# Performance work log

Hardware: AMD Instinct MI355X
Metric: run time of the kernel (lower is better)

The kernel has to match this reference:

```python
import jax, jax.numpy as jnp
import numpy as np

B, T, C, H = 4, 2048, 1024, 16
D = C // H  # head_size = 64


def setup_inputs() -> dict:
    key = jax.random.key(0)
    k1, k2, k3 = jax.random.split(key, 3)
    h = jax.random.normal(k1, (B, T, C), dtype=jnp.float32)
    # additive float mask, [B,1,1,T]; zeros = no padding
    attention_mask = jnp.zeros((B, 1, 1, T), dtype=jnp.float32)
    # learned params (bias=False linears), scaled like default torch init
    w_attn = jax.random.normal(k2, (C, 3 * C), dtype=jnp.float32) / np.sqrt(C)
    w_proj = jax.random.normal(k3, (C, C), dtype=jnp.float32) / np.sqrt(C)
    return {"h": h, "attention_mask": attention_mask, "w_attn": w_attn, "w_proj": w_proj}


def reference(h, attention_mask, w_attn, w_proj):
    # fused QKV projection: [B,T,3C]
    qkv = jnp.einsum("btc,cd->btd", h, w_attn)
    q, k, v = jnp.split(qkv, 3, axis=-1)
    # [B,T,C] -> [B,H,T,D]
    def to_heads(x):
        return x.reshape(B, T, H, D).transpose(0, 2, 1, 3)
    q, k, v = to_heads(q), to_heads(k), to_heads(v)
    # scaled dot-product attention with additive mask (non-causal)
    scale = 1.0 / np.sqrt(D).astype(np.float32)
    scores = jnp.einsum("bhqd,bhkd->bhqk", q, k) * scale + attention_mask
    probs = jax.nn.softmax(scores, axis=-1)
    y = jnp.einsum("bhqk,bhkd->bhqd", probs, v)
    # [B,H,T,D] -> [B,T,C]
    y = y.transpose(0, 2, 1, 3).reshape(B, T, C)
    return jnp.einsum("btc,cd->btd", y, w_proj)
```

## Files before the change

kernel.cpp:

```cpp
#include <hip/hip_runtime.h>
#include <hip/hip_bf16.h>

#define DEV static __device__ __forceinline__

typedef __attribute__((ext_vector_type(4))) float f32x4;
typedef __attribute__((ext_vector_type(16))) float f32x16;
typedef __attribute__((ext_vector_type(8))) short bf16x8;

constexpr int Bb = 4, Ts = 2048, Cc = 1024, Hh = 16, Dd = 64;
constexpr int Mm = Bb * Ts;
constexpr float SCQ = 0.18033688f;

union frag_u {
  bf16x8 f;
  uint2  u2[2];
  ushort us[8];
  uint4  u4;
};

DEV ushort f2bf(float x) {
  union { float f; unsigned u; } v; v.f = x;
  unsigned r = v.u + 0x7FFFu + ((v.u >> 16) & 1u);
  return (ushort)(r >> 16);
}

DEV ushort f2bf_hw(float x) {
  union { __hip_bfloat16 b; ushort u; } cv;
  cv.b = __float2bfloat16(x);
  return cv.u;
}

typedef const __attribute__((address_space(1))) unsigned int gu32;
typedef __attribute__((address_space(3))) unsigned int lu32;
DEV void gload16(const void* g, void* l) {
  __builtin_amdgcn_global_load_lds((gu32*)g, (lu32*)l, 16, 0, 0);
}

DEV void ld_frag16(frag_u& fr, const ushort* lds, int row, int chunk) {
  int off = row * 128 + ((chunk ^ (row & 7)) << 4);
  fr.u4 = *reinterpret_cast<const uint4*>(reinterpret_cast<const char*>(lds) + off);
}
DEV void lds_st64p(ushort* lds, int row, int p, uint2 v) {
  int off = row * 128 + ((((p >> 3) ^ (row & 7)) << 4) | ((2 * p) & 15));
  *reinterpret_cast<uint2*>(reinterpret_cast<char*>(lds) + off) = v;
}

DEV void eW64b(char* E, int row, int col, uint2 v) {
  int off = row * 256 + ((((col >> 3) ^ (row & 15)) << 4) | ((col & 7) * 2));
  *reinterpret_cast<uint2*>(E + off) = v;
}
DEV uint4 eR128b(const char* E, int row, int dc) {
  int off = row * 256 + ((dc ^ (row & 15)) << 4);
  return *reinterpret_cast<const uint4*>(E + off);
}

__global__ __launch_bounds__(256) void cvt_kernel(const float* __restrict__ in,
                                                  ushort* __restrict__ out, int n4) {
  for (int i = blockIdx.x * blockDim.x + threadIdx.x; i < n4;
       i += gridDim.x * blockDim.x) {
    float4 v = reinterpret_cast<const float4*>(in)[i];
    ushort4 o;
    o.x = f2bf(v.x); o.y = f2bf(v.y); o.z = f2bf(v.z); o.w = f2bf(v.w);
    reinterpret_cast<ushort4*>(out)[i] = o;
  }
}

__global__ __launch_bounds__(256) void expmask_kernel(const float* __restrict__ m,
                                                      float* __restrict__ em, int n) {
  int i = blockIdx.x * blockDim.x + threadIdx.x;
  if (i < n) em[i] = __expf(m[i]);
}

__global__ __launch_bounds__(256) void transpose_cvt(const float* __restrict__ in,
                                                     ushort* __restrict__ out,
                                                     int R, int Ccols) {
  __shared__ float tile[32][33];
  int c0 = blockIdx.x * 32, r0 = blockIdx.y * 32;
  int tx = threadIdx.x & 31, ty = threadIdx.x >> 5;
#pragma unroll
  for (int i = 0; i < 4; ++i) {
    int r = ty + i * 8;
    tile[r][tx] = in[(size_t)(r0 + r) * Ccols + c0 + tx];
  }
  __syncthreads();
#pragma unroll
  for (int i = 0; i < 4; ++i) {
    int r = ty + i * 8;
    out[(size_t)(c0 + r) * R + r0 + tx] = f2bf(tile[tx][r]);
  }
}

template <int EPI>
__global__ __launch_bounds__(256) void gemm_bt(const ushort* __restrict__ A,
                                               const ushort* __restrict__ Bt,
                                               int M, int N, int K,
                                               float* __restrict__ Cf,
                                               ushort* __restrict__ Qb,
                                               ushort* __restrict__ Kb,
                                               ushort* __restrict__ Vb,
                                               const float* __restrict__ expm) {
  __shared__ ushort Lds[2][128 * 64];
  __shared__ float evals[128];
  ushort* Al = Lds[0];
  ushort* Bl = Lds[1];
  const int tid = threadIdx.x;
  const int lane = tid & 63, wid = tid >> 6;
  const int l31 = lane & 31, lh = lane >> 5;
  const int wr = wid >> 1, wc = wid & 1;
  const int m0 = blockIdx.y * 128, n0 = blockIdx.x * 128;

  if (EPI == 1 && tid < 128)
    evals[tid] = expm[(size_t)(m0 >> 11) * Ts + (m0 & 2047) + tid];

  f32x16 acc[2][2];
#pragma unroll
  for (int mi = 0; mi < 2; ++mi)
#pragma unroll
    for (int nj = 0; nj < 2; ++nj)
#pragma unroll
      for (int r = 0; r < 16; ++r) acc[mi][nj][r] = 0.f;

  const int nkt = K >> 6;
  for (int kt = 0; kt < nkt; ++kt) {
#pragma unroll
    for (int it = 0; it < 4; ++it) {
      int chunk = wid * 256 + it * 64 + lane;
      int row = chunk >> 3, c16 = (chunk & 7) ^ (row & 7);
      gload16(A + (size_t)(m0 + row) * K + kt * 64 + c16 * 8,
              Al + (size_t)(wid * 256 + it * 64) * 8);
      gload16(Bt + (size_t)(n0 + row) * K + kt * 64 + c16 * 8,
              Bl + (size_t)(wid * 256 + it * 64) * 8);
    }
    __syncthreads();
#pragma unroll
    for (int kk = 0; kk < 4; ++kk) {
      const int chunk = kk * 2 + lh;
      frag_u af[2], bfr[2];
#pragma unroll
      for (int mi = 0; mi < 2; ++mi)
        ld_frag16(af[mi], Al, wr * 64 + mi * 32 + l31, chunk);
#pragma unroll
      for (int nj = 0; nj < 2; ++nj)
        ld_frag16(bfr[nj], Bl, wc * 64 + nj * 32 + l31, chunk);
#pragma unroll
      for (int mi = 0; mi < 2; ++mi)
#pragma unroll
        for (int nj = 0; nj < 2; ++nj)
          acc[mi][nj] = __builtin_amdgcn_mfma_f32_32x32x16_bf16(
              af[mi].f, bfr[nj].f, acc[mi][nj], 0, 0, 0);
    }
    __syncthreads();
  }

  if (EPI == 0) {
#pragma unroll
    for (int mi = 0; mi < 2; ++mi)
#pragma unroll
      for (int nj = 0; nj < 2; ++nj) {
        int ncol = n0 + wc * 64 + nj * 32 + l31;
#pragma unroll
        for (int r = 0; r < 16; ++r) {
          int mrow = m0 + wr * 64 + mi * 32 + (r & 3) + 8 * (r >> 2) + 4 * lh;
          Cf[(size_t)mrow * N + ncol] = acc[mi][nj][r];
        }
      }
  } else {
    const int seg = n0 >> 10;
    const int hd0 = (n0 & 1023) >> 6;
    const int bq = m0 >> 11, tt0 = m0 & 2047;
    if (seg < 2) {
      const float vs = (seg == 0) ? SCQ : 1.0f;
      ushort* dstQ = (seg == 0) ? Qb : Kb;
#pragma unroll
      for (int mi = 0; mi < 2; ++mi)
#pragma unroll
        for (int nj = 0; nj < 2; ++nj) {
          int colb = wc * 64 + nj * 32 + l31;
          int hd = hd0 + (colb >> 6), d = colb & 63;
          ushort* gb = dstQ + (size_t)(bq * Hh + hd) * Ts * Dd + d;
#pragma unroll
          for (int r = 0; r < 16; ++r) {
            int tt = tt0 + wr * 64 + mi * 32 + (r & 3) + 8 * (r >> 2) + 4 * lh;
            gb[(size_t)tt * Dd] = f2bf(acc[mi][nj][r] * vs);
          }
        }
    } else {
      char* E = reinterpret_cast<char*>(&Lds[0][0]);
#pragma unroll
      for (int mi = 0; mi < 2; ++mi)
#pragma unroll
        for (int nj = 0; nj < 2; ++nj) {
          int erow = wc * 64 + nj * 32 + l31;
#pragma unroll
          for (int q2 = 0; q2 < 4; ++q2) {
            int tb = wr * 64 + mi * 32 + 8 * q2 + 4 * lh;
            float e0 = evals[tb], e1 = evals[tb + 1];
            float e2 = evals[tb + 2], e3 = evals[tb + 3];
            unsigned lo = (unsigned)f2bf(acc[mi][nj][4 * q2 + 0] * e0) |
                          ((unsigned)f2bf(acc[mi][nj][4 * q2 + 1] * e1) << 16);
            unsigned hi = (unsigned)f2bf(acc[mi][nj][4 * q2 + 2] * e2) |
                          ((unsigned)f2bf(acc[mi][nj][4 * q2 + 3] * e3) << 16);
            eW64b(E, erow, tb, uint2{lo, hi});
          }
        }
      __syncthreads();
#pragma unroll
      for (int k = 0; k < 8; ++k) {
        int c = k * 256 + tid;
        int row = c >> 4, t16 = c & 15;
        int hd = hd0 + (row >> 6), d = row & 63;
        uint4 v = eR128b(E, row, t16);
        *reinterpret_cast<uint4*>(
            Vb + ((size_t)(bq * Hh + hd) * Dd + d) * Ts + tt0 + t16 * 8) = v;
      }
    }
  }
}

__global__ __launch_bounds__(512, 4) void attn_kernel(const ushort* __restrict__ Qb,
                                                      const ushort* __restrict__ Kb,
                                                      const ushort* __restrict__ VTb,
                                                      const float* __restrict__ expm,
                                                      ushort* __restrict__ Yb) {
  __shared__ ushort Klds[2][64 * 64];
  __shared__ ushort Vlds[2][64 * 64];
  __shared__ ushort wlds[2][64];

  const int tid = threadIdx.x;
  const int lane = tid & 63, wid = tid >> 6;
  const int g = lane >> 4, l15 = lane & 15;
  const int bh = blockIdx.x;
  const int b = bh >> 4, h = bh & 15;
  const int qt = blockIdx.y;

  const ushort* Qh = Qb + (size_t)bh * Ts * Dd;
  const ushort* Kh = Kb + (size_t)bh * Ts * Dd;
  const ushort* Vh = VTb + (size_t)bh * Dd * Ts;
  const float* erow = expm + (size_t)b * Ts;

  const int krow = tid >> 3, kpos = tid & 7;
  const int kc16 = kpos ^ (krow & 7);
  const int srow = tid >> 3, sc16 = tid & 7;
  const int vp0 = 32 * (sc16 >> 2) + 16 * (sc16 & 1) + 4 * ((sc16 >> 1) & 1);
  const int wp = (tid & 32) | ((tid & 12) << 1) | ((tid & 16) >> 2) | (tid & 3);

  frag_u aq[2][2];
#pragma unroll
  for (int qsub = 0; qsub < 2; ++qsub) {
    const ushort* qp = Qh + (size_t)(qt * 256 + wid * 32 + qsub * 16 + l15) * Dd;
#pragma unroll
    for (int ks = 0; ks < 2; ++ks)
      aq[qsub][ks].u4 = *reinterpret_cast<const uint4*>(qp + ks * 32 + 8 * g);
  }

  f32x4 acc[2][4];
  f32x4 lacc[2];
#pragma unroll
  for (int q = 0; q < 2; ++q) {
    lacc[q] = f32x4{0.f, 0.f, 0.f, 0.f};
#pragma unroll
    for (int dt = 0; dt < 4; ++dt) acc[q][dt] = f32x4{0.f, 0.f, 0.f, 0.f};
  }

  uint4 vreg;
  float wreg = 0.f;

#define ISSUE(kt, buf)                                                          \
  gload16(Kh + (size_t)((kt) * 64 + krow) * Dd + kc16 * 8,                      \
          Klds[buf] + (size_t)(wid * 64) * 8);                                  \
  vreg = *reinterpret_cast<const uint4*>(Vh + (size_t)srow * Ts + (kt) * 64 + sc16 * 8); \
  wreg = (tid < 64) ? erow[(kt) * 64 + tid] : 0.f;

#define COMMIT(buf)                                                             \
  lds_st64p(Vlds[buf], srow, vp0, uint2{vreg.x, vreg.y});                       \
  lds_st64p(Vlds[buf], srow, vp0 + 8, uint2{vreg.z, vreg.w});                   \
  if (tid < 64) wlds[buf][wp] = f2bf_hw(wreg);

  ISSUE(0, 0);
  COMMIT(0);
  __syncthreads();

  const int NT = Ts / 64;
  for (int kt = 0; kt < NT; ++kt) {
    const int cur = kt & 1;
    const bool more = (kt + 1 < NT);
    if (more) { ISSUE(kt + 1, cur ^ 1); }

    f32x4 s[2][4];
#pragma unroll
    for (int q = 0; q < 2; ++q)
#pragma unroll
      for (int n = 0; n < 4; ++n) s[q][n] = f32x4{0.f, 0.f, 0.f, 0.f};
    __builtin_amdgcn_s_setprio(1);
#pragma unroll
    for (int ks = 0; ks < 2; ++ks)
#pragma unroll
      for (int n = 0; n < 4; ++n) {
        frag_u bk;
        ld_frag16(bk, Klds[cur], n * 16 + l15, 4 * ks + g);
#pragma unroll
        for (int q = 0; q < 2; ++q)
          s[q][n] = __builtin_amdgcn_mfma_f32_16x16x32_bf16(bk.f, aq[q][ks].f,
                                                            s[q][n], 0, 0, 0);
      }
    __builtin_amdgcn_s_setprio(0);

    frag_u pa[2][2];
#pragma unroll
    for (int q = 0; q < 2; ++q)
#pragma unroll
      for (int n = 0; n < 4; ++n)
#pragma unroll
        for (int r = 0; r < 4; ++r)
          pa[q][n >> 1].us[(n & 1) * 4 + r] =
              f2bf_hw(__builtin_amdgcn_exp2f(s[q][n][r]));

    frag_u wf[2];
    wf[0].u4 = *reinterpret_cast<const uint4*>(&wlds[cur][8 * g]);
    wf[1].u4 = *reinterpret_cast<const uint4*>(&wlds[cur][32 + 8 * g]);
    __builtin_amdgcn_s_setprio(1);
#pragma unroll
    for (int ks = 0; ks < 2; ++ks)
#pragma unroll
      for (int q = 0; q < 2; ++q)
        lacc[q] = __builtin_amdgcn_mfma_f32_16x16x32_bf16(pa[q][ks].f, wf[ks].f,
                                                          lacc[q], 0, 0, 0);
#pragma unroll
    for (int ks = 0; ks < 2; ++ks)
#pragma unroll
      for (int dt = 0; dt < 4; ++dt) {
        frag_u bv;
        ld_frag16(bv, Vlds[cur], dt * 16 + l15, 4 * ks + g);
#pragma unroll
        for (int q = 0; q < 2; ++q)
          acc[q][dt] = __builtin_amdgcn_mfma_f32_16x16x32_bf16(pa[q][ks].f, bv.f,
                                                               acc[q][dt], 0, 0, 0);
      }
    __builtin_amdgcn_s_setprio(0);

    if (more) { COMMIT(cur ^ 1); }
    __syncthreads();
  }
#undef ISSUE
#undef COMMIT

#pragma unroll
  for (int q = 0; q < 2; ++q) {
#pragma unroll
    for (int r = 0; r < 4; ++r) {
      float inv = 1.0f / lacc[q][r];
      int t = qt * 256 + wid * 32 + q * 16 + 4 * g + r;
      size_t base = ((size_t)(b * Ts + t)) * Cc + h * Dd;
#pragma unroll
      for (int dt = 0; dt < 4; ++dt)
        Yb[base + dt * 16 + l15] = f2bf(acc[q][dt][r] * inv);
    }
  }
}

extern "C" void kernel_launch(void* const* d_in, const int* in_sizes, int n_in,
                              void* d_out, int out_size, void* d_ws, size_t ws_size,
                              hipStream_t stream) {
  const float* h    = (const float*)d_in[0];
  const float* mask = (const float*)d_in[1];
  const float* wa   = (const float*)d_in[2];
  const float* wp   = (const float*)d_in[3];
  float* out = (float*)d_out;

  char* ws = (char*)d_ws;
  ushort* hbf     = (ushort*)(ws);
  ushort* wattn_t = (ushort*)(ws + (16u << 20));
  ushort* wproj_t = (ushort*)(ws + (22u << 20));
  ushort* Qb      = (ushort*)(ws + (24u << 20));
  ushort* Kb      = (ushort*)(ws + (40u << 20));
  ushort* VTb     = (ushort*)(ws + (56u << 20));
  float*  expm    = (float*)(ws + (72u << 20));
  ushort* Ybf = hbf;

  cvt_kernel<<<2048, 256, 0, stream>>>(h, hbf, (Mm * Cc) / 4);
  expmask_kernel<<<(Bb * Ts + 255) / 256, 256, 0, stream>>>(mask, expm, Bb * Ts);
  transpose_cvt<<<dim3(3 * Cc / 32, Cc / 32), 256, 0, stream>>>(wa, wattn_t, Cc, 3 * Cc);
  transpose_cvt<<<dim3(Cc / 32, Cc / 32), 256, 0, stream>>>(wp, wproj_t, Cc, Cc);

  gemm_bt<1><<<dim3(3 * Cc / 128, Mm / 128), 256, 0, stream>>>(
      hbf, wattn_t, Mm, 3 * Cc, Cc, nullptr, Qb, Kb, VTb, expm);

  attn_kernel<<<dim3(Bb * Hh, Ts / 256), 512, 0, stream>>>(Qb, Kb, VTb, expm, Ybf);

  gemm_bt<0><<<dim3(Cc / 128, Mm / 128), 256, 0, stream>>>(
      Ybf, wproj_t, Mm, Cc, Cc, out, nullptr, nullptr, nullptr, nullptr);
}
```

Before: 172.1 us.

## Halve attention block to 4 waves, each handling 64 query rows

The attention kernel now launches 256 threads (4 waves) per 256-query tile instead of 8 waves, so each wave processes 64 query rows instead of 32. K fragments are loaded from LDS once per tile into registers and reused across four query sub-blocks, and V LDS fragments are likewise reused across four query groups. Each thread now loads two K and two V chunks per tile. The aim is to cut LDS read traffic per MFMA and the number of waves contending for barriers. The cost is a much larger register footprint, which lowers occupancy and leaves fewer waves to hide latency.

```diff
diff --git a/kernel.cpp b/kernel.cpp
--- a/kernel.cpp
+++ b/kernel.cpp
@@ -217,7 +217,7 @@
   }
 }
 
-__global__ __launch_bounds__(512, 4) void attn_kernel(const ushort* __restrict__ Qb,
+__global__ __launch_bounds__(256, 2) void attn_kernel(const ushort* __restrict__ Qb,
                                                       const ushort* __restrict__ Kb,
                                                       const ushort* __restrict__ VTb,
                                                       const float* __restrict__ expm,
@@ -238,42 +238,48 @@
   const ushort* Vh = VTb + (size_t)bh * Dd * Ts;
   const float* erow = expm + (size_t)b * Ts;
 
-  const int krow = tid >> 3, kpos = tid & 7;
-  const int kc16 = kpos ^ (krow & 7);
+  const int kch0 = tid, kch1 = tid + 256;
+  const int kr0 = kch0 >> 3, kc0 = (kch0 & 7) ^ (kr0 & 7);
+  const int kr1 = kch1 >> 3, kc1 = (kch1 & 7) ^ (kr1 & 7);
   const int srow = tid >> 3, sc16 = tid & 7;
   const int vp0 = 32 * (sc16 >> 2) + 16 * (sc16 & 1) + 4 * ((sc16 >> 1) & 1);
   const int wp = (tid & 32) | ((tid & 12) << 1) | ((tid & 16) >> 2) | (tid & 3);
 
-  frag_u aq[2][2];
-#pragma unroll
-  for (int qsub = 0; qsub < 2; ++qsub) {
-    const ushort* qp = Qh + (size_t)(qt * 256 + wid * 32 + qsub * 16 + l15) * Dd;
+  frag_u aq[4][2];
+#pragma unroll
+  for (int qsub = 0; qsub < 4; ++qsub) {
+    const ushort* qp = Qh + (size_t)(qt * 256 + wid * 64 + qsub * 16 + l15) * Dd;
 #pragma unroll
     for (int ks = 0; ks < 2; ++ks)
       aq[qsub][ks].u4 = *reinterpret_cast<const uint4*>(qp + ks * 32 + 8 * g);
   }
 
-  f32x4 acc[2][4];
-  f32x4 lacc[2];
-#pragma unroll
-  for (int q = 0; q < 2; ++q) {
+  f32x4 acc[4][4];
+  f32x4 lacc[4];
+#pragma unroll
+  for (int q = 0; q < 4; ++q) {
     lacc[q] = f32x4{0.f, 0.f, 0.f, 0.f};
 #pragma unroll
     for (int dt = 0; dt < 4; ++dt) acc[q][dt] = f32x4{0.f, 0.f, 0.f, 0.f};
   }
 
-  uint4 vreg;
+  uint4 vreg0, vreg1;
   float wreg = 0.f;
 
 #define ISSUE(kt, buf)                                                          \
-  gload16(Kh + (size_t)((kt) * 64 + krow) * Dd + kc16 * 8,                      \
+  gload16(Kh + (size_t)((kt) * 64 + kr0) * Dd + kc0 * 8,                        \
           Klds[buf] + (size_t)(wid * 64) * 8);                                  \
-  vreg = *reinterpret_cast<const uint4*>(Vh + (size_t)srow * Ts + (kt) * 64 + sc16 * 8); \
+  gload16(Kh + (size_t)((kt) * 64 + kr1) * Dd + kc1 * 8,                        \
+          Klds[buf] + (size_t)(256 + wid * 64) * 8);                            \
+  vreg0 = *reinterpret_cast<const uint4*>(Vh + (size_t)srow * Ts + (kt) * 64 + sc16 * 8); \
+  vreg1 = *reinterpret_cast<const uint4*>(Vh + (size_t)(srow + 32) * Ts + (kt) * 64 + sc16 * 8); \
   wreg = (tid < 64) ? erow[(kt) * 64 + tid] : 0.f;
 
 #define COMMIT(buf)                                                             \
-  lds_st64p(Vlds[buf], srow, vp0, uint2{vreg.x, vreg.y});                       \
-  lds_st64p(Vlds[buf], srow, vp0 + 8, uint2{vreg.z, vreg.w});                   \
+  lds_st64p(Vlds[buf], srow, vp0, uint2{vreg0.x, vreg0.y});                     \
+  lds_st64p(Vlds[buf], srow, vp0 + 8, uint2{vreg0.z, vreg0.w});                 \
+  lds_st64p(Vlds[buf], srow + 32, vp0, uint2{vreg1.x, vreg1.y});                \
+  lds_st64p(Vlds[buf], srow + 32, vp0 + 8, uint2{vreg1.z, vreg1.w});            \
   if (tid < 64) wlds[buf][wp] = f2bf_hw(wreg);
 
   ISSUE(0, 0);
@@ -286,34 +292,34 @@
     const bool more = (kt + 1 < NT);
     if (more) { ISSUE(kt + 1, cur ^ 1); }
 
-    f32x4 s[2][4];
-#pragma unroll
-    for (int q = 0; q < 2; ++q)
-#pragma unroll
-      for (int n = 0; n < 4; ++n) s[q][n] = f32x4{0.f, 0.f, 0.f, 0.f};
-    __builtin_amdgcn_s_setprio(1);
+    frag_u bkf[2][4];
 #pragma unroll
     for (int ks = 0; ks < 2; ++ks)
 #pragma unroll
-      for (int n = 0; n < 4; ++n) {
-        frag_u bk;
-        ld_frag16(bk, Klds[cur], n * 16 + l15, 4 * ks + g);
-#pragma unroll
-        for (int q = 0; q < 2; ++q)
-          s[q][n] = __builtin_amdgcn_mfma_f32_16x16x32_bf16(bk.f, aq[q][ks].f,
-                                                            s[q][n], 0, 0, 0);
-      }
-    __builtin_amdgcn_s_setprio(0);
-
-    frag_u pa[2][2];
-#pragma unroll
-    for (int q = 0; q < 2; ++q)
+      for (int n = 0; n < 4; ++n)
+        ld_frag16(bkf[ks][n], Klds[cur], n * 16 + l15, 4 * ks + g);
+
+    frag_u pa[4][2];
+#pragma unroll
+    for (int q = 0; q < 4; ++q) {
+      f32x4 s[4];
+#pragma unroll
+      for (int n = 0; n < 4; ++n) s[n] = f32x4{0.f, 0.f, 0.f, 0.f};
+      __builtin_amdgcn_s_setprio(1);
+#pragma unroll
+      for (int ks = 0; ks < 2; ++ks)
+#pragma unroll
+        for (int n = 0; n < 4; ++n)
+          s[n] = __builtin_amdgcn_mfma_f32_16x16x32_bf16(bkf[ks][n].f,
+                                                         aq[q][ks].f, s[n], 0, 0, 0);
+      __builtin_amdgcn_s_setprio(0);
 #pragma unroll
       for (int n = 0; n < 4; ++n)
 #pragma unroll
         for (int r = 0; r < 4; ++r)
           pa[q][n >> 1].us[(n & 1) * 4 + r] =
-              f2bf_hw(__builtin_amdgcn_exp2f(s[q][n][r]));
+              f2bf_hw(__builtin_amdgcn_exp2f(s[n][r]));
+    }
 
     frag_u wf[2];
     wf[0].u4 = *reinterpret_cast<const uint4*>(&wlds[cur][8 * g]);
@@ -322,7 +328,7 @@
 #pragma unroll
     for (int ks = 0; ks < 2; ++ks)
 #pragma unroll
-      for (int q = 0; q < 2; ++q)
+      for (int q = 0; q < 4; ++q)
         lacc[q] = __builtin_amdgcn_mfma_f32_16x16x32_bf16(pa[q][ks].f, wf[ks].f,
                                                           lacc[q], 0, 0, 0);
 #pragma unroll
@@ -332,7 +338,7 @@
         frag_u bv;
         ld_frag16(bv, Vlds[cur], dt * 16 + l15, 4 * ks + g);
 #pragma unroll
-        for (int q = 0; q < 2; ++q)
+        for (int q = 0; q < 4; ++q)
           acc[q][dt] = __builtin_amdgcn_mfma_f32_16x16x32_bf16(pa[q][ks].f, bv.f,
                                                                acc[q][dt], 0, 0, 0);
       }
@@ -345,11 +351,11 @@
 #undef COMMIT
 
 #pragma unroll
-  for (int q = 0; q < 2; ++q) {
+  for (int q = 0; q < 4; ++q) {
 #pragma unroll
     for (int r = 0; r < 4; ++r) {
       float inv = 1.0f / lacc[q][r];
-      int t = qt * 256 + wid * 32 + q * 16 + 4 * g + r;
+      int t = qt * 256 + wid * 64 + q * 16 + 4 * g + r;
       size_t base = ((size_t)(b * Ts + t)) * Cc + h * Dd;
 #pragma unroll
       for (int dt = 0; dt < 4; ++dt)
@@ -385,7 +391,7 @@
   gemm_bt<1><<<dim3(3 * Cc / 128, Mm / 128), 256, 0, stream>>>(
       hbf, wattn_t, Mm, 3 * Cc, Cc, nullptr, Qb, Kb, VTb, expm);
 
-  attn_kernel<<<dim3(Bb * Hh, Ts / 256), 512, 0, stream>>>(Qb, Kb, VTb, expm, Ybf);
+  attn_kernel<<<dim3(Bb * Hh, Ts / 256), 256, 0, stream>>>(Qb, Kb, VTb, expm, Ybf);
 
   gemm_bt<0><<<dim3(Cc / 128, Mm / 128), 256, 0, stream>>>(
       Ybf, wproj_t, Mm, Cc, Cc, out, nullptr, nullptr, nullptr, nullptr);
```

Result: no change. 173.1 us (+0.5%).
